# Optimization experiments

Measured on AMD Instinct MI355X. Metric: run time of the kernel, lower is better.

Reference implementation:

```python
import jax, jax.numpy as jnp
import numpy as np

BN_EPS = 1e-5

def _batchnorm(z, gamma, beta):
    # training-mode BN over node axis, biased variance (matches torch normalization)
    mean = jnp.mean(z, axis=0)
    var = jnp.mean((z - mean) ** 2, axis=0)
    return (z - mean) * jax.lax.rsqrt(var + BN_EPS) * gamma + beta

def setup_inputs() -> dict:
    key = jax.random.key(0)
    N, E, D, L = 100000, 1000000, 128, 2
    ks = jax.random.split(key, 8)
    x = jax.random.normal(ks[0], (N, D), dtype=jnp.float32)
    edge_index = jax.random.randint(ks[1], (2, E), 0, N, dtype=jnp.int64)
    s = 1.0 / np.sqrt(D)
    W1 = jax.random.uniform(ks[2], (L, D, D), jnp.float32, -s, s)
    b1 = jax.random.uniform(ks[3], (L, D), jnp.float32, -s, s)
    W2 = jax.random.uniform(ks[4], (L, D, D), jnp.float32, -s, s)
    b2 = jax.random.uniform(ks[5], (L, D), jnp.float32, -s, s)
    g1 = jnp.ones((L, D), jnp.float32); bt1 = jnp.zeros((L, D), jnp.float32)
    g_out = jnp.ones((L, D), jnp.float32); bt_out = jnp.zeros((L, D), jnp.float32)
    eps = jnp.zeros((L,), jnp.float32)  # GIN eps, init 0
    return {"x": x, "edge_index": edge_index, "W1": W1, "b1": b1, "g1": g1,
            "bt1": bt1, "W2": W2, "b2": b2, "eps": eps, "g_out": g_out, "bt_out": bt_out}

def reference(x, edge_index, W1, b1, g1, bt1, W2, b2, eps, g_out, bt_out):
    N = x.shape[0]
    L = W1.shape[0]
    src, dst = edge_index[0], edge_index[1]
    h = x
    for l in range(L):
        # message: relu(x_j) gathered along edges; aggregate: scatter-add to dst
        msg = jax.nn.relu(h[src])                                  # [E, D]
        aggr = jax.ops.segment_sum(msg, dst, num_segments=N)       # [N, D]
        z = (1.0 + eps[l]) * h + aggr
        # GINConv MLP: Linear -> BN -> ReLU -> Linear
        z = z @ W1[l].T + b1[l]
        z = jax.nn.relu(_batchnorm(z, g1[l], bt1[l]))
        z = z @ W2[l].T + b2[l]
        # outer per-layer BatchNorm
        z = _batchnorm(z, g_out[l], bt_out[l])
        if l < L - 1:
            z = jax.nn.relu(z)
        # dropout is identity in eval mode
        h = z
    return h
```

## Files before the change

kernel.cpp:

```cpp
#include <hip/hip_runtime.h>

typedef unsigned int u32;
typedef unsigned short u16;
typedef __attribute__((ext_vector_type(8))) short bf16x8;
typedef __attribute__((ext_vector_type(4))) float f32x4;

#define DF 128
#define NBUCK 256
#define BUCK_SHIFT 9
#define BUCK_SIZE 512
#define P2_CHUNK 4096
#define NCOPY 16
#define STATW (NCOPY * DF)

__device__ __forceinline__ float bf2f(u32 h) { return __uint_as_float(h << 16); }
__device__ __forceinline__ u16 f2bf(float f) {
  u32 u = __float_as_uint(f);
  u32 r = (u + 0x7fffu + ((u >> 16) & 1u)) >> 16;
  return (u16)r;
}
__device__ __forceinline__ u32 pack2(float a, float b) {
  return (u32)f2bf(a) | ((u32)f2bf(b) << 16);
}

__global__ void k_cvt_f32_bf16(const float* __restrict__ in, u16* __restrict__ out, int n4) {
  int i = blockIdx.x * blockDim.x + threadIdx.x;
  if (i >= n4) return;
  float4 v = ((const float4*)in)[i];
  ((uint2*)out)[i] = make_uint2(pack2(v.x, v.y), pack2(v.z, v.w));
}

__global__ __launch_bounds__(256) void k_p1(const int* __restrict__ dst,
                                            int* __restrict__ bucketCount, int E) {
  __shared__ int h[NBUCK];
  int t = threadIdx.x;
  h[t] = 0;
  __syncthreads();
  for (int e = blockIdx.x * 256 + t; e < E; e += gridDim.x * 256)
    atomicAdd(&h[((u32)dst[e]) >> BUCK_SHIFT], 1);
  __syncthreads();
  if (h[t]) atomicAdd(&bucketCount[t], h[t]);
}

__global__ __launch_bounds__(256) void k_pscan(const int* __restrict__ bucketCount,
                                               int* __restrict__ bucketStart,
                                               int* __restrict__ bucketCursor,
                                               int* __restrict__ rowptr, int N, int E) {
  __shared__ int sh[NBUCK];
  int t = threadIdx.x;
  int c = bucketCount[t];
  sh[t] = c;
  __syncthreads();
  for (int o = 1; o < 256; o <<= 1) {
    int v = (t >= o) ? sh[t - o] : 0;
    __syncthreads();
    sh[t] += v;
    __syncthreads();
  }
  int excl = sh[t] - c;
  bucketStart[t] = excl;
  bucketCursor[t] = excl;
  if (t == 255) { bucketStart[256] = sh[255]; rowptr[N] = E; }
}

__global__ __launch_bounds__(256) void k_p2(const int* __restrict__ src,
                                            const int* __restrict__ dst,
                                            int* __restrict__ bucketCursor,
                                            uint2* __restrict__ part, int E) {
  __shared__ int h[NBUCK], hs[NBUCK], base[NBUCK];
  __shared__ int total;
  __shared__ uint2 buf[P2_CHUNK];
  int t = threadIdx.x;
  int e0 = blockIdx.x * P2_CHUNK;
  h[t] = 0;
  __syncthreads();
  int myb[16], myr[16];
  uint2 mye[16];
  #pragma unroll
  for (int k = 0; k < 16; k++) {
    int e = e0 + k * 256 + t;
    myb[k] = -1;
    if (e < E) {
      int s = src[e], d = dst[e];
      mye[k] = make_uint2((u32)s, (u32)d);
      myb[k] = ((u32)d) >> BUCK_SHIFT;
      myr[k] = atomicAdd(&h[myb[k]], 1);
    }
  }
  __syncthreads();
  int hc = h[t];
  hs[t] = hc;
  __syncthreads();
  for (int o = 1; o < 256; o <<= 1) {
    int v = (t >= o) ? hs[t - o] : 0;
    __syncthreads();
    hs[t] += v;
    __syncthreads();
  }
  if (t == 255) total = hs[255];
  int excl = hs[t] - hc;
  base[t] = hc ? atomicAdd(&bucketCursor[t], hc) : 0;
  __syncthreads();
  hs[t] = excl;
  __syncthreads();
  #pragma unroll
  for (int k = 0; k < 16; k++)
    if (myb[k] >= 0) buf[hs[myb[k]] + myr[k]] = mye[k];
  __syncthreads();
  int tot = total;
  for (int i = t; i < tot; i += 256) {
    uint2 ed = buf[i];
    int b = ed.y >> BUCK_SHIFT;
    part[base[b] + (i - hs[b])] = ed;
  }
}

__global__ __launch_bounds__(256) void k_p3(const uint2* __restrict__ part,
                                            const int* __restrict__ bucketStart,
                                            int* __restrict__ rowptr,
                                            int* __restrict__ adj, int N) {
  __shared__ int deg[BUCK_SIZE], cur[BUCK_SIZE], psum[256];
  int b = blockIdx.x, t = threadIdx.x;
  int nodeBase = b << BUCK_SHIFT;
  int eb = bucketStart[b], ee = bucketStart[b + 1];
  deg[t] = 0; deg[t + 256] = 0;
  __syncthreads();
  for (int e = eb + t; e < ee; e += 256)
    atomicAdd(&deg[(int)part[e].y - nodeBase], 1);
  __syncthreads();
  int a0 = deg[2 * t], a1 = deg[2 * t + 1];
  psum[t] = a0 + a1;
  __syncthreads();
  for (int o = 1; o < 256; o <<= 1) {
    int v = (t >= o) ? psum[t - o] : 0;
    __syncthreads();
    psum[t] += v;
    __syncthreads();
  }
  int basep = psum[t] - (a0 + a1);
  int p0 = eb + basep, p1 = eb + basep + a0;
  cur[2 * t] = p0; cur[2 * t + 1] = p1;
  int n0 = nodeBase + 2 * t, n1 = nodeBase + 2 * t + 1;
  if (n0 < N) rowptr[n0] = p0;
  if (n1 < N) rowptr[n1] = p1;
  __syncthreads();
  for (int e = eb + t; e < ee; e += 256) {
    uint2 ed = part[e];
    int pos = atomicAdd(&cur[(int)ed.y - nodeBase], 1);
    adj[pos] = (int)ed.x;
  }
}

__global__ void k_aggr(const u16* __restrict__ hin,
                       const int* __restrict__ rowptr, const int* __restrict__ adj,
                       const float* __restrict__ epsArr, int layer,
                       const float* __restrict__ aAff, const float* __restrict__ cAff,
                       int selfRelu,
                       u16* __restrict__ z, int N) {
  int wid = (blockIdx.x * blockDim.x + threadIdx.x) >> 6;
  if (wid >= N) return;
  int lane = threadIdx.x & 63;
  int g = lane >> 4, f = lane & 15;
  const uint4* h4 = (const uint4*)hin;
  float e1 = 1.0f + epsArr[layer];

  float av[8], cv[8];
  if (aAff) {
    float4 a0 = *(const float4*)(aAff + f * 8);
    float4 a1 = *(const float4*)(aAff + f * 8 + 4);
    float4 c0 = *(const float4*)(cAff + f * 8);
    float4 c1 = *(const float4*)(cAff + f * 8 + 4);
    av[0] = a0.x; av[1] = a0.y; av[2] = a0.z; av[3] = a0.w;
    av[4] = a1.x; av[5] = a1.y; av[6] = a1.z; av[7] = a1.w;
    cv[0] = c0.x; cv[1] = c0.y; cv[2] = c0.z; cv[3] = c0.w;
    cv[4] = c1.x; cv[5] = c1.y; cv[6] = c1.z; cv[7] = c1.w;
  } else {
    #pragma unroll
    for (int k = 0; k < 8; k++) { av[k] = 1.0f; cv[k] = 0.0f; }
  }

  float acc[8];
  #pragma unroll
  for (int k = 0; k < 8; k++) acc[k] = 0.0f;

  if (g == 0) {
    uint4 v = h4[(size_t)wid * 16 + f];
    u32 w[4] = {v.x, v.y, v.z, v.w};
    #pragma unroll
    for (int k = 0; k < 4; k++) {
      float lo = fmaf(av[2 * k],     __uint_as_float(w[k] << 16),         cv[2 * k]);
      float hi = fmaf(av[2 * k + 1], __uint_as_float(w[k] & 0xffff0000u), cv[2 * k + 1]);
      if (selfRelu) { lo = fmaxf(lo, 0.0f); hi = fmaxf(hi, 0.0f); }
      acc[2 * k]     = e1 * lo;
      acc[2 * k + 1] = e1 * hi;
    }
  }

  int b = rowptr[wid], e = rowptr[wid + 1];
  int inv = 0;
  for (int p = b; p < e; p += 8) {
    int i0 = p + g, i1 = p + 4 + g;
    uint4 v0 = make_uint4(0, 0, 0, 0), v1 = make_uint4(0, 0, 0, 0);
    if (i0 < e) v0 = h4[(size_t)(u32)adj[i0] * 16 + f]; else inv++;
    if (i1 < e) v1 = h4[(size_t)(u32)adj[i1] * 16 + f]; else inv++;
    u32 w0[4] = {v0.x, v0.y, v0.z, v0.w};
    u32 w1[4] = {v1.x, v1.y, v1.z, v1.w};
    #pragma unroll
    for (int k = 0; k < 4; k++) {
      acc[2 * k]     += fmaxf(fmaf(av[2 * k],     __uint_as_float(w0[k] << 16),         cv[2 * k]),     0.0f);
      acc[2 * k + 1] += fmaxf(fmaf(av[2 * k + 1], __uint_as_float(w0[k] & 0xffff0000u), cv[2 * k + 1]), 0.0f);
      acc[2 * k]     += fmaxf(fmaf(av[2 * k],     __uint_as_float(w1[k] << 16),         cv[2 * k]),     0.0f);
      acc[2 * k + 1] += fmaxf(fmaf(av[2 * k + 1], __uint_as_float(w1[k] & 0xffff0000u), cv[2 * k + 1]), 0.0f);
    }
  }
  float cinv = (float)inv;
  #pragma unroll
  for (int k = 0; k < 8; k++) acc[k] -= cinv * fmaxf(cv[k], 0.0f);

  #pragma unroll
  for (int k = 0; k < 8; k++) {
    acc[k] += __shfl_xor(acc[k], 16);
    acc[k] += __shfl_xor(acc[k], 32);
  }
  if (g == 0) {
    uint4 o = make_uint4(pack2(acc[0], acc[1]), pack2(acc[2], acc[3]),
                         pack2(acc[4], acc[5]), pack2(acc[6], acc[7]));
    ((uint4*)z)[(size_t)wid * 16 + f] = o;
  }
}

__global__ __launch_bounds__(256, 2) void k_gemm(
    const u16* __restrict__ A, const u16* __restrict__ W, const float* __restrict__ bias,
    const float* __restrict__ Sprev, const float* __restrict__ Qprev,
    const float* __restrict__ gprev, const float* __restrict__ btprev, int trans,
    float* __restrict__ statS, float* __restrict__ statQ,
    u16* __restrict__ out, int Nrows) {
  __shared__ u16 lA[4 * 8 * 64 * 8];
  __shared__ u16 lB[4 * 8 * 64 * 8];
  __shared__ float sAf[DF], sCf[DF];
  int tid = threadIdx.x;
  int rowBase = blockIdx.x * 128;

  if (trans) {
    if (tid < DF) {
      float Sv = 0.f, Qv = 0.f;
      #pragma unroll
      for (int i = 0; i < NCOPY; i++) { Sv += Sprev[i * DF + tid]; Qv += Qprev[i * DF + tid]; }
      float inv_n = 1.0f / (float)Nrows;
      float mean = Sv * inv_n;
      float var = fmaxf(Qv * inv_n - mean * mean, 0.0f);
      float iv = rsqrtf(var + 1e-5f);
      float a = gprev[tid] * iv;
      sAf[tid] = a;
      sCf[tid] = btprev[tid] - mean * a;
    }
    __syncthreads();
  }

  #pragma unroll
  for (int cc = 0; cc < 8; cc++) {
    int c = tid + cc * 256;
    int lane = c & 63, rt = (c >> 6) & 7, kt = c >> 9;
    int m = lane & 15, quad = lane >> 4;
    int grow = rowBase + rt * 16 + m;
    int gk = kt * 32 + quad * 8;
    uint4 val = make_uint4(0, 0, 0, 0);
    if (grow < Nrows) val = *(const uint4*)(A + (size_t)grow * DF + gk);
    if (trans) {
      float4 av0 = *(const float4*)(sAf + gk);
      float4 av1 = *(const float4*)(sAf + gk + 4);
      float4 cv0 = *(const float4*)(sCf + gk);
      float4 cv1 = *(const float4*)(sCf + gk + 4);
      float f0 = fmaxf(fmaf(av0.x, bf2f(val.x & 0xffffu), cv0.x), 0.0f);
      float f1 = fmaxf(fmaf(av0.y, bf2f(val.x >> 16),     cv0.y), 0.0f);
      float f2 = fmaxf(fmaf(av0.z, bf2f(val.y & 0xffffu), cv0.z), 0.0f);
      float f3 = fmaxf(fmaf(av0.w, bf2f(val.y >> 16),     cv0.w), 0.0f);
      float f4 = fmaxf(fmaf(av1.x, bf2f(val.z & 0xffffu), cv1.x), 0.0f);
      float f5 = fmaxf(fmaf(av1.y, bf2f(val.z >> 16),     cv1.y), 0.0f);
      float f6 = fmaxf(fmaf(av1.z, bf2f(val.w & 0xffffu), cv1.z), 0.0f);
      float f7 = fmaxf(fmaf(av1.w, bf2f(val.w >> 16),     cv1.w), 0.0f);
      val = make_uint4(pack2(f0, f1), pack2(f2, f3), pack2(f4, f5), pack2(f6, f7));
    }
    ((uint4*)lA)[c] = val;
  }
  #pragma unroll
  for (int cc = 0; cc < 8; cc++) {
    int c = tid + cc * 256;
    int lane = c & 63, ct = (c >> 6) & 7, kt = c >> 9;
    int n = lane & 15, quad = lane >> 4;
    ((uint4*)lB)[c] = *(const uint4*)(W + (ct * 16 + n) * DF + kt * 32 + quad * 8);
  }
  __syncthreads();

  int lane = tid & 63, w = tid >> 6;
  int rq = w >> 1, cq = w & 1;
  f32x4 acc[4][4];
  #pragma unroll
  for (int i = 0; i < 4; i++)
    #pragma unroll
    for (int j = 0; j < 4; j++) acc[i][j] = (f32x4){0.f, 0.f, 0.f, 0.f};

  const bf16x8* pA = (const bf16x8*)lA;
  const bf16x8* pB = (const bf16x8*)lB;
  #pragma unroll
  for (int kt = 0; kt < 4; kt++) {
    bf16x8 af[4], bfr[4];
    #pragma unroll
    for (int i = 0; i < 4; i++) af[i] = pA[(kt * 8 + rq * 4 + i) * 64 + lane];
    #pragma unroll
    for (int j = 0; j < 4; j++) bfr[j] = pB[(kt * 8 + cq * 4 + j) * 64 + lane];
    #pragma unroll
    for (int i = 0; i < 4; i++)
      #pragma unroll
      for (int j = 0; j < 4; j++)
        acc[i][j] = __builtin_amdgcn_mfma_f32_16x16x32_bf16(af[i], bfr[j], acc[i][j], 0, 0, 0);
  }

  int mcol = lane & 15, quad = lane >> 4;
  float colS[4] = {0, 0, 0, 0}, colQ[4] = {0, 0, 0, 0};
  #pragma unroll
  for (int j = 0; j < 4; j++) {
    int col = (cq * 4 + j) * 16 + mcol;
    float bv = bias[col];
    #pragma unroll
    for (int i = 0; i < 4; i++) {
      int row0 = rowBase + (rq * 4 + i) * 16 + quad * 4;
      #pragma unroll
      for (int r = 0; r < 4; r++) {
        int row = row0 + r;
        if (row < Nrows) {
          float v = acc[i][j][r] + bv;
          out[(size_t)row * DF + col] = f2bf(v);
          colS[j] += v;
          colQ[j] += v * v;
        }
      }
    }
  }
  int copyOff = (blockIdx.x & (NCOPY - 1)) * DF;
  #pragma unroll
  for (int j = 0; j < 4; j++) {
    float s = colS[j], q = colQ[j];
    s += __shfl_xor(s, 16); q += __shfl_xor(q, 16);
    s += __shfl_xor(s, 32); q += __shfl_xor(q, 32);
    if (quad == 0) {
      int col = (cq * 4 + j) * 16 + mcol;
      atomicAdd(&statS[copyOff + col], s);
      atomicAdd(&statQ[copyOff + col], q);
    }
  }
}

__global__ void k_finalize(const float* __restrict__ s, const float* __restrict__ q,
                           const float* __restrict__ gamma, const float* __restrict__ beta,
                           float* __restrict__ a, float* __restrict__ c, int Nrows) {
  int t = threadIdx.x;
  if (t < DF) {
    float S = 0.f, Q = 0.f;
    #pragma unroll
    for (int i = 0; i < NCOPY; i++) { S += s[i * DF + t]; Q += q[i * DF + t]; }
    float inv_n = 1.0f / (float)Nrows;
    float mean = S * inv_n;
    float var = fmaxf(Q * inv_n - mean * mean, 0.0f);
    float iv = rsqrtf(var + 1e-5f);
    float av = gamma[t] * iv;
    a[t] = av;
    c[t] = beta[t] - mean * av;
  }
}

__global__ __launch_bounds__(256) void k_bnout_f32(
    const u16* __restrict__ u, const float* __restrict__ S, const float* __restrict__ Q,
    const float* __restrict__ gamma, const float* __restrict__ beta, int Nrows,
    float* __restrict__ out, int n8) {
  __shared__ float sAf[DF], sCf[DF];
  int tid = threadIdx.x;
  if (tid < DF) {
    float Sv = 0.f, Qv = 0.f;
    #pragma unroll
    for (int i = 0; i < NCOPY; i++) { Sv += S[i * DF + tid]; Qv += Q[i * DF + tid]; }
    float inv_n = 1.0f / (float)Nrows;
    float mean = Sv * inv_n;
    float var = fmaxf(Qv * inv_n - mean * mean, 0.0f);
    float iv = rsqrtf(var + 1e-5f);
    float a = gamma[tid] * iv;
    sAf[tid] = a;
    sCf[tid] = beta[tid] - mean * a;
  }
  __syncthreads();
  for (int i = blockIdx.x * 256 + tid; i < n8; i += gridDim.x * 256) {
    int col = (i * 8) & 127;
    float4 a0 = *(const float4*)(sAf + col), a1v = *(const float4*)(sAf + col + 4);
    float4 c0 = *(const float4*)(sCf + col), c1v = *(const float4*)(sCf + col + 4);
    uint4 v = ((const uint4*)u)[i];
    float4 o0, o1;
    o0.x = fmaf(a0.x, bf2f(v.x & 0xffffu), c0.x);
    o0.y = fmaf(a0.y, bf2f(v.x >> 16),     c0.y);
    o0.z = fmaf(a0.z, bf2f(v.y & 0xffffu), c0.z);
    o0.w = fmaf(a0.w, bf2f(v.y >> 16),     c0.w);
    o1.x = fmaf(a1v.x, bf2f(v.z & 0xffffu), c1v.x);
    o1.y = fmaf(a1v.y, bf2f(v.z >> 16),     c1v.y);
    o1.z = fmaf(a1v.z, bf2f(v.w & 0xffffu), c1v.z);
    o1.w = fmaf(a1v.w, bf2f(v.w >> 16),     c1v.w);
    ((float4*)out)[i * 2] = o0;
    ((float4*)out)[i * 2 + 1] = o1;
  }
}

extern "C" void kernel_launch(void* const* d_in, const int* in_sizes, int n_in,
                              void* d_out, int out_size, void* d_ws, size_t ws_size,
                              hipStream_t stream) {
  const float* x    = (const float*)d_in[0];
  const int*   ei   = (const int*)d_in[1];
  const float* W1   = (const float*)d_in[2];
  const float* b1   = (const float*)d_in[3];
  const float* g1   = (const float*)d_in[4];
  const float* bt1  = (const float*)d_in[5];
  const float* W2   = (const float*)d_in[6];
  const float* b2   = (const float*)d_in[7];
  const float* eps  = (const float*)d_in[8];
  const float* gout = (const float*)d_in[9];
  const float* btout= (const float*)d_in[10];

  int N = in_sizes[0] / DF;
  int E = in_sizes[1] / 2;
  int L = in_sizes[8];

  char* ws = (char*)d_ws;
  size_t off = 0;
  auto alloc = [&](size_t bytes) -> void* {
    void* p = ws + off;
    off += (bytes + 255) & ~(size_t)255;
    return p;
  };
  u16* Xb     = (u16*)alloc((size_t)N * DF * 2);
  u16* bufA   = (u16*)alloc((size_t)N * DF * 2);
  u16* bufB   = (u16*)alloc((size_t)N * DF * 2);
  int* rowptr = (int*)alloc((size_t)(N + 1) * 4);
  int* adj    = (int*)alloc((size_t)E * 4);
  uint2* part = (uint2*)alloc((size_t)E * 8);
  int* bCount = (int*)alloc(NBUCK * 4);
  int* bStart = (int*)alloc((NBUCK + 1) * 4);
  int* bCur   = (int*)alloc(NBUCK * 4);
  u16* W1b    = (u16*)alloc((size_t)L * DF * DF * 2);
  u16* W2b    = (u16*)alloc((size_t)L * DF * DF * 2);
  float* stats= (float*)alloc((size_t)L * 4 * STATW * 4);
  float* coefs= (float*)alloc((size_t)L * 4 * DF * 4);

  hipMemsetAsync(bCount, 0, NBUCK * 4, stream);
  hipMemsetAsync(stats, 0, (size_t)L * 4 * STATW * 4, stream);

  int n4x = N * DF / 4;
  k_cvt_f32_bf16<<<(n4x + 255) / 256, 256, 0, stream>>>(x, Xb, n4x);
  int n4w = L * DF * DF / 4;
  k_cvt_f32_bf16<<<(n4w + 255) / 256, 256, 0, stream>>>(W1, W1b, n4w);
  k_cvt_f32_bf16<<<(n4w + 255) / 256, 256, 0, stream>>>(W2, W2b, n4w);

  const int* srcI = ei;
  const int* dstI = ei + E;
  int nbuckets = (N + BUCK_SIZE - 1) >> BUCK_SHIFT;
  k_p1<<<512, 256, 0, stream>>>(dstI, bCount, E);
  k_pscan<<<1, 256, 0, stream>>>(bCount, bStart, bCur, rowptr, N, E);
  k_p2<<<(E + P2_CHUNK - 1) / P2_CHUNK, 256, 0, stream>>>(srcI, dstI, bCur, part, E);
  k_p3<<<nbuckets, 256, 0, stream>>>(part, bStart, rowptr, adj, N);

  int gblocks = (N + 127) / 128;
  int n8 = N * DF / 8;
  const u16* Hcur = Xb;
  const float* aPrev = nullptr;
  const float* cPrev = nullptr;
  int selfRelu = 0;
  for (int l = 0; l < L; l++) {
    float* S1 = stats + (size_t)(l * 4 + 0) * STATW;
    float* Q1 = stats + (size_t)(l * 4 + 1) * STATW;
    float* S2 = stats + (size_t)(l * 4 + 2) * STATW;
    float* Q2 = stats + (size_t)(l * 4 + 3) * STATW;
    float* a2 = coefs + (size_t)(l * 4 + 2) * DF;
    float* c2 = coefs + (size_t)(l * 4 + 3) * DF;
    u16* z = (l & 1) ? bufB : bufA;
    u16* t = (l & 1) ? bufA : bufB;
    u16* u = z;

    k_aggr<<<(N + 3) / 4, 256, 0, stream>>>(Hcur, rowptr, adj, eps, l,
                                            aPrev, cPrev, selfRelu, z, N);
    k_gemm<<<gblocks, 256, 0, stream>>>(z, W1b + l * DF * DF, b1 + l * DF,
                                        nullptr, nullptr, nullptr, nullptr, 0,
                                        S1, Q1, t, N);
    k_gemm<<<gblocks, 256, 0, stream>>>(t, W2b + l * DF * DF, b2 + l * DF,
                                        S1, Q1, g1 + l * DF, bt1 + l * DF, 1,
                                        S2, Q2, u, N);
    if (l < L - 1) {
      k_finalize<<<1, 128, 0, stream>>>(S2, Q2, gout + l * DF, btout + l * DF, a2, c2, N);
      aPrev = a2; cPrev = c2; selfRelu = 1;
      Hcur = u;
    } else {
      k_bnout_f32<<<2048, 256, 0, stream>>>(u, S2, Q2, gout + l * DF, btout + l * DF,
                                            N, (float*)d_out, n8);
    }
  }
}
```

Before: 429.9 us.

## Switch activations to fp16 with packed-half aggregation and LDS-staged GEMM stores

```diff
diff --git a/kernel.cpp b/kernel.cpp
--- a/kernel.cpp
+++ b/kernel.cpp
@@ -1,8 +1,9 @@
 #include <hip/hip_runtime.h>
+#include <hip/hip_fp16.h>
 
 typedef unsigned int u32;
 typedef unsigned short u16;
-typedef __attribute__((ext_vector_type(8))) short bf16x8;
+typedef __attribute__((ext_vector_type(8))) _Float16 f16x8;
 typedef __attribute__((ext_vector_type(4))) float f32x4;
 
 #define DF 128
@@ -12,22 +13,26 @@
 #define P2_CHUNK 4096
 #define NCOPY 16
 #define STATW (NCOPY * DF)
-
-__device__ __forceinline__ float bf2f(u32 h) { return __uint_as_float(h << 16); }
-__device__ __forceinline__ u16 f2bf(float f) {
-  u32 u = __float_as_uint(f);
-  u32 r = (u + 0x7fffu + ((u >> 16) & 1u)) >> 16;
-  return (u16)r;
-}
-__device__ __forceinline__ u32 pack2(float a, float b) {
-  return (u32)f2bf(a) | ((u32)f2bf(b) << 16);
-}
-
-__global__ void k_cvt_f32_bf16(const float* __restrict__ in, u16* __restrict__ out, int n4) {
+#define CSTRIDE 132
+
+__device__ __forceinline__ __half2 u2h2(u32 x) { union { u32 u; __half2 h; } v; v.u = x; return v.h; }
+__device__ __forceinline__ u32 h22u(__half2 h) { union { u32 u; __half2 h; } v; v.h = h; return v.u; }
+__device__ __forceinline__ u32 pack2h(float a, float b) { return h22u(__floats2half2_rn(a, b)); }
+
+__device__ __forceinline__ u32 pkmax_u(u32 a, u32 b) {
+  u32 r;
+  asm("v_pk_max_f16 %0, %1, %2" : "=v"(r) : "v"(a), "v"(b));
+  return r;
+}
+__device__ __forceinline__ __half2 hmax2(__half2 a, __half2 b) {
+  return u2h2(pkmax_u(h22u(a), h22u(b)));
+}
+
+__global__ void k_cvt_f32_f16(const float* __restrict__ in, u16* __restrict__ out, int n4) {
   int i = blockIdx.x * blockDim.x + threadIdx.x;
   if (i >= n4) return;
   float4 v = ((const float4*)in)[i];
-  ((uint2*)out)[i] = make_uint2(pack2(v.x, v.y), pack2(v.z, v.w));
+  ((uint2*)out)[i] = make_uint2(pack2h(v.x, v.y), pack2h(v.z, v.w));
 }
 
 __global__ __launch_bounds__(256) void k_p1(const int* __restrict__ dst,
@@ -163,6 +168,7 @@
   int g = lane >> 4, f = lane & 15;
   const uint4* h4 = (const uint4*)hin;
   float e1 = 1.0f + epsArr[layer];
+  __half2 zero2 = __floats2half2_rn(0.0f, 0.0f);
 
   float av[8], cv[8];
   if (aAff) {
@@ -178,22 +184,13 @@
     #pragma unroll
     for (int k = 0; k < 8; k++) { av[k] = 1.0f; cv[k] = 0.0f; }
   }
-
-  float acc[8];
-  #pragma unroll
-  for (int k = 0; k < 8; k++) acc[k] = 0.0f;
-
-  if (g == 0) {
-    uint4 v = h4[(size_t)wid * 16 + f];
-    u32 w[4] = {v.x, v.y, v.z, v.w};
-    #pragma unroll
-    for (int k = 0; k < 4; k++) {
-      float lo = fmaf(av[2 * k],     __uint_as_float(w[k] << 16),         cv[2 * k]);
-      float hi = fmaf(av[2 * k + 1], __uint_as_float(w[k] & 0xffff0000u), cv[2 * k + 1]);
-      if (selfRelu) { lo = fmaxf(lo, 0.0f); hi = fmaxf(hi, 0.0f); }
-      acc[2 * k]     = e1 * lo;
-      acc[2 * k + 1] = e1 * hi;
-    }
+  __half2 a2[4], c2[4], cm2[4], acc2[4];
+  #pragma unroll
+  for (int k = 0; k < 4; k++) {
+    a2[k] = __floats2half2_rn(av[2 * k], av[2 * k + 1]);
+    c2[k] = __floats2half2_rn(cv[2 * k], cv[2 * k + 1]);
+    cm2[k] = hmax2(c2[k], zero2);
+    acc2[k] = zero2;
   }
 
   int b = rowptr[wid], e = rowptr[wid + 1];
@@ -207,25 +204,32 @@
     u32 w1[4] = {v1.x, v1.y, v1.z, v1.w};
     #pragma unroll
     for (int k = 0; k < 4; k++) {
-      acc[2 * k]     += fmaxf(fmaf(av[2 * k],     __uint_as_float(w0[k] << 16),         cv[2 * k]),     0.0f);
-      acc[2 * k + 1] += fmaxf(fmaf(av[2 * k + 1], __uint_as_float(w0[k] & 0xffff0000u), cv[2 * k + 1]), 0.0f);
-      acc[2 * k]     += fmaxf(fmaf(av[2 * k],     __uint_as_float(w1[k] << 16),         cv[2 * k]),     0.0f);
-      acc[2 * k + 1] += fmaxf(fmaf(av[2 * k + 1], __uint_as_float(w1[k] & 0xffff0000u), cv[2 * k + 1]), 0.0f);
-    }
-  }
-  float cinv = (float)inv;
-  #pragma unroll
-  for (int k = 0; k < 8; k++) acc[k] -= cinv * fmaxf(cv[k], 0.0f);
-
-  #pragma unroll
-  for (int k = 0; k < 8; k++) {
-    acc[k] += __shfl_xor(acc[k], 16);
-    acc[k] += __shfl_xor(acc[k], 32);
-  }
+      acc2[k] = __hadd2(acc2[k], hmax2(__hfma2(a2[k], u2h2(w0[k]), c2[k]), zero2));
+      acc2[k] = __hadd2(acc2[k], hmax2(__hfma2(a2[k], u2h2(w1[k]), c2[k]), zero2));
+    }
+  }
+  __half2 inv2 = __floats2half2_rn((float)inv, (float)inv);
+  #pragma unroll
+  for (int k = 0; k < 4; k++) {
+    acc2[k] = __hsub2(acc2[k], __hmul2(inv2, cm2[k]));
+    acc2[k] = __hadd2(acc2[k], u2h2(__shfl_xor(h22u(acc2[k]), 16)));
+    acc2[k] = __hadd2(acc2[k], u2h2(__shfl_xor(h22u(acc2[k]), 32)));
+  }
+
   if (g == 0) {
-    uint4 o = make_uint4(pack2(acc[0], acc[1]), pack2(acc[2], acc[3]),
-                         pack2(acc[4], acc[5]), pack2(acc[6], acc[7]));
-    ((uint4*)z)[(size_t)wid * 16 + f] = o;
+    uint4 sv = h4[(size_t)wid * 16 + f];
+    u32 sw[4] = {sv.x, sv.y, sv.z, sv.w};
+    u32 o[4];
+    #pragma unroll
+    for (int k = 0; k < 4; k++) {
+      float2 s = __half22float2(u2h2(sw[k]));
+      float lo = fmaf(av[2 * k], s.x, cv[2 * k]);
+      float hi = fmaf(av[2 * k + 1], s.y, cv[2 * k + 1]);
+      if (selfRelu) { lo = fmaxf(lo, 0.0f); hi = fmaxf(hi, 0.0f); }
+      float2 nb = __half22float2(acc2[k]);
+      o[k] = pack2h(fmaf(e1, lo, nb.x), fmaf(e1, hi, nb.y));
+    }
+    ((uint4*)z)[(size_t)wid * 16 + f] = make_uint4(o[0], o[1], o[2], o[3]);
   }
 }
 
@@ -235,24 +239,35 @@
     const float* __restrict__ gprev, const float* __restrict__ btprev, int trans,
     float* __restrict__ statS, float* __restrict__ statQ,
     u16* __restrict__ out, int Nrows) {
-  __shared__ u16 lA[4 * 8 * 64 * 8];
-  __shared__ u16 lB[4 * 8 * 64 * 8];
-  __shared__ float sAf[DF], sCf[DF];
+  __shared__ __align__(16) char smem[128 * CSTRIDE * 4 + 512];
+  u16* lA = (u16*)smem;
+  u16* lB = (u16*)(smem + 32768);
+  float* sC = (float*)smem;
+  __half2* sA2 = (__half2*)(smem + 128 * CSTRIDE * 4);
+  __half2* sC2 = (__half2*)(smem + 128 * CSTRIDE * 4 + 256);
   int tid = threadIdx.x;
   int rowBase = blockIdx.x * 128;
+  __half2 zero2 = __floats2half2_rn(0.0f, 0.0f);
 
   if (trans) {
-    if (tid < DF) {
-      float Sv = 0.f, Qv = 0.f;
+    if (tid < 64) {
+      float aa[2], cc[2];
       #pragma unroll
-      for (int i = 0; i < NCOPY; i++) { Sv += Sprev[i * DF + tid]; Qv += Qprev[i * DF + tid]; }
-      float inv_n = 1.0f / (float)Nrows;
-      float mean = Sv * inv_n;
-      float var = fmaxf(Qv * inv_n - mean * mean, 0.0f);
-      float iv = rsqrtf(var + 1e-5f);
-      float a = gprev[tid] * iv;
-      sAf[tid] = a;
-      sCf[tid] = btprev[tid] - mean * a;
+      for (int j = 0; j < 2; j++) {
+        int col = tid * 2 + j;
+        float Sv = 0.f, Qv = 0.f;
+        #pragma unroll
+        for (int i = 0; i < NCOPY; i++) { Sv += Sprev[i * DF + col]; Qv += Qprev[i * DF + col]; }
+        float inv_n = 1.0f / (float)Nrows;
+        float mean = Sv * inv_n;
+        float var = fmaxf(Qv * inv_n - mean * mean, 0.0f);
+        float iv = rsqrtf(var + 1e-5f);
+        float a = gprev[col] * iv;
+        aa[j] = a;
+        cc[j] = btprev[col] - mean * a;
+      }
+      sA2[tid] = __floats2half2_rn(aa[0], aa[1]);
+      sC2[tid] = __floats2half2_rn(cc[0], cc[1]);
     }
     __syncthreads();
   }
@@ -267,19 +282,12 @@
     uint4 val = make_uint4(0, 0, 0, 0);
     if (grow < Nrows) val = *(const uint4*)(A + (size_t)grow * DF + gk);
     if (trans) {
-      float4 av0 = *(const float4*)(sAf + gk);
-      float4 av1 = *(const float4*)(sAf + gk + 4);
-      float4 cv0 = *(const float4*)(sCf + gk);
-      float4 cv1 = *(const float4*)(sCf + gk + 4);
-      float f0 = fmaxf(fmaf(av0.x, bf2f(val.x & 0xffffu), cv0.x), 0.0f);
-      float f1 = fmaxf(fmaf(av0.y, bf2f(val.x >> 16),     cv0.y), 0.0f);
-      float f2 = fmaxf(fmaf(av0.z, bf2f(val.y & 0xffffu), cv0.z), 0.0f);
-      float f3 = fmaxf(fmaf(av0.w, bf2f(val.y >> 16),     cv0.w), 0.0f);
-      float f4 = fmaxf(fmaf(av1.x, bf2f(val.z & 0xffffu), cv1.x), 0.0f);
-      float f5 = fmaxf(fmaf(av1.y, bf2f(val.z >> 16),     cv1.y), 0.0f);
-      float f6 = fmaxf(fmaf(av1.z, bf2f(val.w & 0xffffu), cv1.z), 0.0f);
-      float f7 = fmaxf(fmaf(av1.w, bf2f(val.w >> 16),     cv1.w), 0.0f);
-      val = make_uint4(pack2(f0, f1), pack2(f2, f3), pack2(f4, f5), pack2(f6, f7));
+      uint4 aw = ((const uint4*)sA2)[gk >> 3];
+      uint4 cw = ((const uint4*)sC2)[gk >> 3];
+      val.x = pkmax_u(h22u(__hfma2(u2h2(aw.x), u2h2(val.x), u2h2(cw.x))), 0u);
+      val.y = pkmax_u(h22u(__hfma2(u2h2(aw.y), u2h2(val.y), u2h2(cw.y))), 0u);
+      val.z = pkmax_u(h22u(__hfma2(u2h2(aw.z), u2h2(val.z), u2h2(cw.z))), 0u);
+      val.w = pkmax_u(h22u(__hfma2(u2h2(aw.w), u2h2(val.w), u2h2(cw.w))), 0u);
     }
     ((uint4*)lA)[c] = val;
   }
@@ -300,11 +308,11 @@
     #pragma unroll
     for (int j = 0; j < 4; j++) acc[i][j] = (f32x4){0.f, 0.f, 0.f, 0.f};
 
-  const bf16x8* pA = (const bf16x8*)lA;
-  const bf16x8* pB = (const bf16x8*)lB;
+  const f16x8* pA = (const f16x8*)lA;
+  const f16x8* pB = (const f16x8*)lB;
   #pragma unroll
   for (int kt = 0; kt < 4; kt++) {
-    bf16x8 af[4], bfr[4];
+    f16x8 af[4], bfr[4];
     #pragma unroll
     for (int i = 0; i < 4; i++) af[i] = pA[(kt * 8 + rq * 4 + i) * 64 + lane];
     #pragma unroll
@@ -313,8 +321,10 @@
     for (int i = 0; i < 4; i++)
       #pragma unroll
       for (int j = 0; j < 4; j++)
-        acc[i][j] = __builtin_amdgcn_mfma_f32_16x16x32_bf16(af[i], bfr[j], acc[i][j], 0, 0, 0);
-  }
+        acc[i][j] = __builtin_amdgcn_mfma_f32_16x16x32_f16(af[i], bfr[j], acc[i][j], 0, 0, 0);
+  }
+
+  __syncthreads();
 
   int mcol = lane & 15, quad = lane >> 4;
   float colS[4] = {0, 0, 0, 0}, colQ[4] = {0, 0, 0, 0};
@@ -324,19 +334,33 @@
     float bv = bias[col];
     #pragma unroll
     for (int i = 0; i < 4; i++) {
-      int row0 = rowBase + (rq * 4 + i) * 16 + quad * 4;
+      int rel0 = (rq * 4 + i) * 16 + quad * 4;
       #pragma unroll
       for (int r = 0; r < 4; r++) {
-        int row = row0 + r;
-        if (row < Nrows) {
-          float v = acc[i][j][r] + bv;
-          out[(size_t)row * DF + col] = f2bf(v);
-          colS[j] += v;
-          colQ[j] += v * v;
-        }
+        int rel = rel0 + r;
+        float v = acc[i][j][r] + bv;
+        sC[rel * CSTRIDE + col] = v;
+        if (rowBase + rel < Nrows) { colS[j] += v; colQ[j] += v * v; }
       }
     }
   }
+  __syncthreads();
+
+  #pragma unroll
+  for (int k = 0; k < 8; k++) {
+    int idx = k * 256 + tid;
+    int rel = idx >> 4;
+    int c0 = (idx & 15) * 8;
+    int row = rowBase + rel;
+    if (row < Nrows) {
+      float4 x0 = *(const float4*)(sC + rel * CSTRIDE + c0);
+      float4 x1 = *(const float4*)(sC + rel * CSTRIDE + c0 + 4);
+      uint4 o = make_uint4(pack2h(x0.x, x0.y), pack2h(x0.z, x0.w),
+                           pack2h(x1.x, x1.y), pack2h(x1.z, x1.w));
+      *(uint4*)(out + (size_t)row * DF + c0) = o;
+    }
+  }
+
   int copyOff = (blockIdx.x & (NCOPY - 1)) * DF;
   #pragma unroll
   for (int j = 0; j < 4; j++) {
@@ -393,15 +417,19 @@
     float4 a0 = *(const float4*)(sAf + col), a1v = *(const float4*)(sAf + col + 4);
     float4 c0 = *(const float4*)(sCf + col), c1v = *(const float4*)(sCf + col + 4);
     uint4 v = ((const uint4*)u)[i];
+    float2 f0 = __half22float2(u2h2(v.x));
+    float2 f1 = __half22float2(u2h2(v.y));
+    float2 f2 = __half22float2(u2h2(v.z));
+    float2 f3 = __half22float2(u2h2(v.w));
     float4 o0, o1;
-    o0.x = fmaf(a0.x, bf2f(v.x & 0xffffu), c0.x);
-    o0.y = fmaf(a0.y, bf2f(v.x >> 16),     c0.y);
-    o0.z = fmaf(a0.z, bf2f(v.y & 0xffffu), c0.z);
-    o0.w = fmaf(a0.w, bf2f(v.y >> 16),     c0.w);
-    o1.x = fmaf(a1v.x, bf2f(v.z & 0xffffu), c1v.x);
-    o1.y = fmaf(a1v.y, bf2f(v.z >> 16),     c1v.y);
-    o1.z = fmaf(a1v.z, bf2f(v.w & 0xffffu), c1v.z);
-    o1.w = fmaf(a1v.w, bf2f(v.w >> 16),     c1v.w);
+    o0.x = fmaf(a0.x, f0.x, c0.x);
+    o0.y = fmaf(a0.y, f0.y, c0.y);
+    o0.z = fmaf(a0.z, f1.x, c0.z);
+    o0.w = fmaf(a0.w, f1.y, c0.w);
+    o1.x = fmaf(a1v.x, f2.x, c1v.x);
+    o1.y = fmaf(a1v.y, f2.y, c1v.y);
+    o1.z = fmaf(a1v.z, f3.x, c1v.z);
+    o1.w = fmaf(a1v.w, f3.y, c1v.w);
     ((float4*)out)[i * 2] = o0;
     ((float4*)out)[i * 2 + 1] = o1;
   }
@@ -451,10 +479,10 @@
   hipMemsetAsync(stats, 0, (size_t)L * 4 * STATW * 4, stream);
 
   int n4x = N * DF / 4;
-  k_cvt_f32_bf16<<<(n4x + 255) / 256, 256, 0, stream>>>(x, Xb, n4x);
+  k_cvt_f32_f16<<<(n4x + 255) / 256, 256, 0, stream>>>(x, Xb, n4x);
   int n4w = L * DF * DF / 4;
-  k_cvt_f32_bf16<<<(n4w + 255) / 256, 256, 0, stream>>>(W1, W1b, n4w);
-  k_cvt_f32_bf16<<<(n4w + 255) / 256, 256, 0, stream>>>(W2, W2b, n4w);
+  k_cvt_f32_f16<<<(n4w + 255) / 256, 256, 0, stream>>>(W1, W1b, n4w);
+  k_cvt_f32_f16<<<(n4w + 255) / 256, 256, 0, stream>>>(W2, W2b, n4w);
 
   const int* srcI = ei;
   const int* dstI = ei + E;
```

After: 370.7 us. 13.8% less time.
